# Kernel optimization log

Hardware: AMD Instinct MI355X
Metric: run time of the kernel (lower is better)

Reference implementation:

```python
import jax, jax.numpy as jnp
import numpy as np

B, N, T, E, H = 2, 512, 12, 128, 8
D = E // H  # head_dim = 16


def setup_inputs() -> dict:
    key = jax.random.key(0)
    ks = jax.random.split(key, 16)
    mk = lambda k, shape, s=1.0: (jax.random.normal(k, shape, dtype=jnp.float32) * s)
    inp = {
        'flow_q': mk(ks[0], (B, N, T, E)),
        'flow_k': mk(ks[1], (B, N, T, E)),
        'flow_v': mk(ks[2], (B, N, T, E)),
        'speed_q': mk(ks[3], (B, N, T, E)),
        'speed_k': mk(ks[4], (B, N, T, E)),
        'speed_v': mk(ks[5], (B, N, T, E)),
        # Linear weights stored as (in, out) so y = x @ W
        'WfQ': mk(ks[6], (E, E), 1.0 / np.sqrt(E)),
        'WfK': mk(ks[7], (E, E), 1.0 / np.sqrt(E)),
        'WfV': mk(ks[8], (E, E), 1.0 / np.sqrt(E)),
        'WsQ': mk(ks[9], (E, E), 1.0 / np.sqrt(E)),
        'WsK': mk(ks[10], (E, E), 1.0 / np.sqrt(E)),
        'WsV': mk(ks[11], (E, E), 1.0 / np.sqrt(E)),
        'Kj': mk(ks[12], (N, 1)),          # FlowSpeed params (xavier ~ small)
        'Vfp': mk(ks[13], (N, 1)),
        'Wout': mk(ks[14], (E, E), 1.0 / np.sqrt(E)),
        'bout': jnp.zeros((E,), dtype=jnp.float32),
    }
    return inp


def _heads(x, W):
    # [B,N,T,C] @ [C,E] -> [B,N,T,H,D] -> [B,H,T,N,D]
    y = jnp.einsum('bntc,ce->bnte', x, W).reshape(B, N, T, H, D)
    return jnp.transpose(y, (0, 3, 2, 1, 4))


def reference(flow_q, flow_k, flow_v, speed_q, speed_k, speed_v,
              WfQ, WfK, WfV, WsQ, WsK, WsV, Kj, Vfp, Wout, bout):
    Qf = _heads(flow_q, WfQ)
    Kf = _heads(flow_k, WfK)
    Vf = _heads(flow_v, WfV)
    Qs = _heads(speed_q, WsQ)
    Ks = _heads(speed_k, WsK)
    Vs = _heads(speed_v, WsV)

    scale = 1.0 / np.sqrt(D)
    # FlowSpeed nonlinearity on Qs; Kj/Vfp (N,1) broadcast over [B,H,T,N,D]
    Qf_from_speed = Kj * (Qs - Qs * Qs / (Vfp + 1e-05))

    att = lambda A, Bm: jax.nn.softmax(
        jnp.einsum('bhtnd,bhtmd->bhtnm', A, Bm) * scale, axis=-1)

    z_ff = att(Qf, Kf)
    z_fs = att(Kf, Qf_from_speed)
    z_sf = att(Ks, Qf)
    z_ss = att(Qs, Ks)

    ctx = lambda z, V: jnp.einsum('bhtnm,bhtmd->bhtnd', z, V)

    def proj_out(c):
        # [B,H,T,N,D] -> [B,N,T,H*D] -> fc_out
        c = jnp.transpose(c, (0, 3, 2, 1, 4)).reshape(B, N, T, E)
        return jnp.einsum('bnte,ef->bntf', c, Wout) + bout

    out_ff = proj_out(ctx(z_ff, Vf))
    out_fs = proj_out(ctx(z_fs, Vf))
    out_sf = proj_out(ctx(z_sf, Vs))
    out_ss = proj_out(ctx(z_ss, Vs))
    return (out_ff, out_fs, out_sf, out_ss)
```

## Files before the change

### kernel.cpp

```cpp
#include <hip/hip_runtime.h>
#include <math.h>

constexpr int Bb = 2, Nn = 512, Tt = 12, Ee = 128, Hh = 8, Dd = 16;
constexpr int NTOK   = Bb * Nn * Tt;
constexpr int PROJ   = NTOK * Ee;
constexpr int SLICES = Bb * Hh * Tt;
constexpr int NSL    = Nn * Dd;
constexpr long SLE   = (long)SLICES * NSL;
constexpr int NSL17  = 17 * 512;
constexpr long SLE17 = (long)SLICES * NSL17;


struct PtrPack { const float* x[6]; const float* W[6]; };
struct WPack   { const float* W[7]; };

typedef __attribute__((ext_vector_type(8)))  short bf16x8;
typedef __attribute__((ext_vector_type(16))) float f32x16;
union FragU { bf16x8 v; unsigned u[4]; };

__device__ __forceinline__ unsigned pk_bf16(float a, float b) {
  unsigned r;
  asm("v_cvt_pk_bf16_f32 %0, %1, %2" : "=v"(r) : "v"(a), "v"(b));
  return r;
}
__device__ __forceinline__ void split_frag(const float e[8], bf16x8& hv, bf16x8& lv) {
  FragU H, L;
  #pragma unroll
  for (int i = 0; i < 4; ++i) {
    const unsigned h = pk_bf16(e[2*i], e[2*i+1]);
    const float h0 = __uint_as_float(h << 16);
    const float h1 = __uint_as_float(h & 0xffff0000u);
    L.u[i] = pk_bf16(e[2*i] - h0, e[2*i+1] - h1);
    H.u[i] = h;
  }
  hv = H.v; lv = L.v;
}

__global__ __launch_bounds__(256) void prep_w_kernel(
    WPack wp, unsigned short* __restrict__ wf)
{
  const int m = blockIdx.x;
  const float SQ = sqrtf(0.25f * 1.4426950408889634f);
  const float scale = (m == 0 || m == 1 || m == 3 || m == 4) ? SQ : 1.0f;
  const float* __restrict__ W = wp.W[m];
  for (int e = threadIdx.x; e < 2048; e += 256) {
    const int ct = e >> 9, ks = (e >> 6) & 7, lane = e & 63;
    const int ql = lane & 31, hi = lane >> 5;
    const int c = ct * 32 + ql, k0 = ks * 16 + hi * 8;
    float w[8];
    #pragma unroll
    for (int j = 0; j < 8; ++j) w[j] = W[(size_t)(k0 + j) * Ee + c] * scale;
    bf16x8 hv, lv;
    split_frag(w, hv, lv);
    *(bf16x8*)&wf[((size_t)(m * 2 + 0) * 2048 + e) * 8] = hv;
    *(bf16x8*)&wf[((size_t)(m * 2 + 1) * 2048 + e) * 8] = lv;
  }
}

__global__ __launch_bounds__(256) void proj_mfma_kernel(
    PtrPack pp, const float* __restrict__ Kj, const float* __restrict__ Vfp,
    unsigned short* __restrict__ qk, unsigned short* __restrict__ vt,
    const unsigned short* __restrict__ wf)
{
  __shared__ float XS[32][132];
  const int ty = blockIdx.y;
  const int g  = blockIdx.x;
  const int nc = g & 15;
  const int bt = g >> 4;
  const int b  = bt / Tt, t = bt % Tt;
  const int n0 = nc * 32;
  const int tid = threadIdx.x;
  const int wave = tid >> 6, lane = tid & 63;
  const int ql = lane & 31, hi = lane >> 5;

  const float* __restrict__ xg = pp.x[ty];
  for (int i = tid; i < 1024; i += 256) {
    const int row = i >> 5, ch = i & 31;
    *(float4*)&XS[row][ch * 4] =
        *(const float4*)&xg[((size_t)(b * Nn + n0 + row) * Tt + t) * Ee + ch * 4];
  }
  __syncthreads();

  f32x16 acc;
  #pragma unroll
  for (int r = 0; r < 16; ++r) acc[r] = 0.f;

  const unsigned short* __restrict__ wbase =
      wf + ((size_t)(ty * 2) * 2048 + wave * 512 + lane) * 8;

  for (int ks = 0; ks < 8; ++ks) {
    float e8[8];
    *(float4*)&e8[0] = *(const float4*)&XS[ql][ks * 16 + hi * 8];
    *(float4*)&e8[4] = *(const float4*)&XS[ql][ks * 16 + hi * 8 + 4];
    bf16x8 xh, xl;
    split_frag(e8, xh, xl);
    const bf16x8 wh = *(const bf16x8*)&wbase[(size_t)ks * 512];
    const bf16x8 wl = *(const bf16x8*)&wbase[(size_t)ks * 512 + 2048 * 8];
    acc = __builtin_amdgcn_mfma_f32_32x32x16_bf16(xh, wh, acc, 0, 0, 0);
    acc = __builtin_amdgcn_mfma_f32_32x32x16_bf16(xh, wl, acc, 0, 0, 0);
    acc = __builtin_amdgcn_mfma_f32_32x32x16_bf16(xl, wh, acc, 0, 0, 0);
    if (ty == 3)
      acc = __builtin_amdgcn_mfma_f32_32x32x16_bf16(xl, wl, acc, 0, 0, 0);
  }
  __syncthreads();

  #pragma unroll
  for (int r = 0; r < 16; ++r)
    XS[(r & 3) + 8 * (r >> 2) + 4 * hi][wave * 32 + ql] = acc[r];
  __syncthreads();

  if (ty == 2 || ty == 5) {
    if (tid < 128) {
      const int h = tid >> 4, d = tid & 15;
      const int slice = (b * Hh + h) * Tt + t;
      const long vsel = (ty == 5);
      float v[32];
      #pragma unroll
      for (int n = 0; n < 32; ++n) v[n] = XS[n][h * 16 + d];
      FragU F[4];
      #pragma unroll
      for (int i = 0; i < 16; ++i)
        F[i >> 2].u[i & 3] = pk_bf16(v[2 * i], v[2 * i + 1]);
      unsigned short* __restrict__ dst =
          vt + vsel * SLE17 + (size_t)slice * NSL17 + d * 512 + n0;
      #pragma unroll
      for (int i = 0; i < 4; ++i) *(bf16x8*)&dst[i * 8] = F[i].v;
      if (d == 0) {
        FragU O_;
        #pragma unroll
        for (int i = 0; i < 4; ++i) O_.u[i] = 0x3F803F80u;
        unsigned short* __restrict__ op =
            vt + vsel * SLE17 + (size_t)slice * NSL17 + 16 * 512 + n0;
        #pragma unroll
        for (int i = 0; i < 4; ++i) *(bf16x8*)&op[i * 8] = O_.v;
      }
    }
  } else {
    const int h = tid >> 5, nn = tid & 31;
    const int slice = (b * Hh + h) * Tt + t;
    const int n = n0 + nn;
    float v[16];
    #pragma unroll
    for (int d = 0; d < 16; ++d) v[d] = XS[nn][h * 16 + d];
    FragU HI[2], LO[2];
    #pragma unroll
    for (int i = 0; i < 8; ++i) {
      const unsigned hw = pk_bf16(v[2 * i], v[2 * i + 1]);
      const float h0 = __uint_as_float(hw << 16);
      const float h1 = __uint_as_float(hw & 0xffff0000u);
      HI[i >> 2].u[i & 3] = hw;
      LO[i >> 2].u[i & 3] = pk_bf16(v[2 * i] - h0, v[2 * i + 1] - h1);
    }
    const int s = (ty == 0) ? 0 : (ty == 1) ? 1 : (ty == 3) ? 2 : 3;
    unsigned short* __restrict__ hp =
        qk + (size_t)(s * 2 + 0) * SLE + (size_t)slice * NSL + n * 16;
    unsigned short* __restrict__ lp =
        qk + (size_t)(s * 2 + 1) * SLE + (size_t)slice * NSL + n * 16;
    *(bf16x8*)&hp[0] = HI[0].v;  *(bf16x8*)&hp[8] = HI[1].v;
    *(bf16x8*)&lp[0] = LO[0].v;  *(bf16x8*)&lp[8] = LO[1].v;
    if (ty == 3) {
      const float SQ  = sqrtf(0.25f * 1.4426950408889634f);
      const float RSQ = 1.0f / SQ;
      const float kj = Kj[n];
      const float iv = 1.0f / (Vfp[n] + 1e-5f);
      float gv[16];
      #pragma unroll
      for (int d = 0; d < 16; ++d) {
        const float vq = v[d] * RSQ;
        gv[d] = SQ * (kj * (vq - vq * vq * iv));
      }
      FragU GH[2], GL[2];
      #pragma unroll
      for (int i = 0; i < 8; ++i) {
        const unsigned hw = pk_bf16(gv[2 * i], gv[2 * i + 1]);
        const float h0 = __uint_as_float(hw << 16);
        const float h1 = __uint_as_float(hw & 0xffff0000u);
        GH[i >> 2].u[i & 3] = hw;
        GL[i >> 2].u[i & 3] = pk_bf16(gv[2 * i] - h0, gv[2 * i + 1] - h1);
      }
      unsigned short* __restrict__ gp =
          qk + (size_t)(4 * 2 + 0) * SLE + (size_t)slice * NSL + n * 16;
      unsigned short* __restrict__ glp =
          qk + (size_t)(4 * 2 + 1) * SLE + (size_t)slice * NSL + n * 16;
      *(bf16x8*)&gp[0]  = GH[0].v;  *(bf16x8*)&gp[8]  = GH[1].v;
      *(bf16x8*)&glp[0] = GL[0].v;  *(bf16x8*)&glp[8] = GL[1].v;
    }
  }
}

__global__ __launch_bounds__(256) void attn_mfma_kernel(
    const unsigned short* __restrict__ qk, const unsigned short* __restrict__ vt,
    unsigned short* __restrict__ ctxh, unsigned short* __restrict__ ctxl)
{
  const int slice = blockIdx.x;
  const int ty    = blockIdx.y;
  const int a_s[4] = {0, 1, 3, 2};
  const int b_s[4] = {1, 4, 0, 3};
  const int v_s[4] = {0, 0, 1, 1};

  const unsigned short* __restrict__ Ah =
      qk + (size_t)(a_s[ty] * 2 + 0) * SLE + (size_t)slice * NSL;
  const unsigned short* __restrict__ Al =
      qk + (size_t)(a_s[ty] * 2 + 1) * SLE + (size_t)slice * NSL;
  const unsigned short* __restrict__ Kh_ =
      qk + (size_t)(b_s[ty] * 2 + 0) * SLE + (size_t)slice * NSL;
  const unsigned short* __restrict__ Kl_ =
      qk + (size_t)(b_s[ty] * 2 + 1) * SLE + (size_t)slice * NSL;
  const unsigned short* __restrict__ Vt_ =
      vt + (size_t)v_s[ty] * SLE17 + (size_t)slice * NSL17;

  const int tid  = threadIdx.x;
  const int wave = tid >> 6;
  const int lane = tid & 63;
  const int hi   = lane >> 5;
  const int ql   = lane & 31;
  const int q0   = blockIdx.z * 256 + wave * 64;
  const int dv   = (ql < 16) ? ql : 16;
  const unsigned short* __restrict__ vbase = Vt_ + dv * 512;

  bf16x8 qh[2], qlo[2];
  #pragma unroll
  for (int qt = 0; qt < 2; ++qt) {
    const int qrow = q0 + qt * 32 + ql;
    qh[qt]  = *(const bf16x8*)&Ah[qrow * 16 + hi * 8];
    qlo[qt] = *(const bf16x8*)&Al[qrow * 16 + hi * 8];
  }

  f32x16 Z;
  #pragma unroll
  for (int r = 0; r < 16; ++r) Z[r] = 0.0f;

  f32x16 o[2];
  float  m_[2] = {-1e30f, -1e30f};
  #pragma unroll
  for (int qt = 0; qt < 2; ++qt)
    #pragma unroll
    for (int r = 0; r < 16; ++r) o[qt][r] = 0.0f;

  for (int kc = 0; kc < Nn; kc += 32) {
    const int krow = kc + ql;
    const bf16x8 kh = *(const bf16x8*)&Kh_[krow * 16 + hi * 8];
    const bf16x8 kl = *(const bf16x8*)&Kl_[krow * 16 + hi * 8];
    const bf16x8 vb0 = *(const bf16x8*)&vbase[kc + hi * 8];
    const bf16x8 vb1 = *(const bf16x8*)&vbase[kc + 16 + hi * 8];

    #pragma unroll
    for (int qt = 0; qt < 2; ++qt) {
      f32x16 S;
      S = __builtin_amdgcn_mfma_f32_32x32x16_bf16(kh, qh[qt],  Z, 0, 0, 0);
      S = __builtin_amdgcn_mfma_f32_32x32x16_bf16(kh, qlo[qt], S, 0, 0, 0);
      S = __builtin_amdgcn_mfma_f32_32x32x16_bf16(kl, qh[qt],  S, 0, 0, 0);
      if (ty == 1)
        S = __builtin_amdgcn_mfma_f32_32x32x16_bf16(kl, qlo[qt], S, 0, 0, 0);

      float p[16];
      if (ty == 1) {
        float smax = S[0];
        #pragma unroll
        for (int r = 1; r < 16; ++r) smax = fmaxf(smax, S[r]);
        float cm = fmaxf(smax, __shfl_xor(smax, 32));
        if (!__all(cm <= m_[qt] + 8.0f)) {
          const float nm = fmaxf(m_[qt], cm);
          const float f  = __builtin_amdgcn_exp2f(m_[qt] - nm);
          #pragma unroll
          for (int r = 0; r < 16; ++r) {
            const int qloc = (r & 3) + 8 * (r >> 2) + 4 * hi;
            o[qt][r] *= __shfl(f, qloc);
          }
          m_[qt] = nm;
        }
        #pragma unroll
        for (int r = 0; r < 16; ++r)
          p[r] = __builtin_amdgcn_exp2f(S[r] - m_[qt]);
      } else {
        #pragma unroll
        for (int r = 0; r < 16; ++r)
          p[r] = __builtin_amdgcn_exp2f(S[r]);
      }

      FragU pa0, pa1;
      {
        unsigned wa = pk_bf16(p[0],  p[1]);
        unsigned wb = pk_bf16(p[2],  p[3]);
        unsigned wc = pk_bf16(p[4],  p[5]);
        unsigned wd = pk_bf16(p[6],  p[7]);
        asm("v_permlane32_swap_b32 %0, %1" : "+v"(wa), "+v"(wc));
        asm("v_permlane32_swap_b32 %0, %1" : "+v"(wb), "+v"(wd));
        pa0.u[0] = wa; pa0.u[1] = wb; pa0.u[2] = wc; pa0.u[3] = wd;
        unsigned we = pk_bf16(p[8],  p[9]);
        unsigned wg = pk_bf16(p[10], p[11]);
        unsigned wi = pk_bf16(p[12], p[13]);
        unsigned wj = pk_bf16(p[14], p[15]);
        asm("v_permlane32_swap_b32 %0, %1" : "+v"(we), "+v"(wi));
        asm("v_permlane32_swap_b32 %0, %1" : "+v"(wg), "+v"(wj));
        pa1.u[0] = we; pa1.u[1] = wg; pa1.u[2] = wi; pa1.u[3] = wj;
      }
      o[qt] = __builtin_amdgcn_mfma_f32_32x32x16_bf16(pa0.v, vb0, o[qt], 0, 0, 0);
      o[qt] = __builtin_amdgcn_mfma_f32_32x32x16_bf16(pa1.v, vb1, o[qt], 0, 0, 0);
    }
  }

  const int b = slice / (Hh * Tt);
  const int h = (slice / Tt) % Hh;
  const int t = slice % Tt;
  unsigned short* __restrict__ ch = ctxh + (size_t)ty * PROJ;
  unsigned short* __restrict__ cl = ctxl + (size_t)ty * PROJ;
  const int lsrc = (lane & 32) | 16;
  #pragma unroll
  for (int qt = 0; qt < 2; ++qt) {
    #pragma unroll
    for (int r = 0; r < 16; ++r) {
      const int qloc = (r & 3) + 8 * (r >> 2) + 4 * hi;
      const float lsum = __shfl(o[qt][r], lsrc);
      if (ql < 16) {
        const int n = q0 + qt * 32 + qloc;
        const float val = o[qt][r] * __builtin_amdgcn_rcpf(lsum);
        const unsigned hv = pk_bf16(val, val);
        const float hf = __uint_as_float(hv << 16);
        const unsigned lv = pk_bf16(val - hf, val - hf);
        const size_t off = (((size_t)b * Nn + n) * Tt + t) * Ee + h * Dd + ql;
        ch[off] = (unsigned short)hv;
        cl[off] = (unsigned short)lv;
      }
    }
  }
}

__global__ __launch_bounds__(256) void out_mfma_kernel(
    const unsigned short* __restrict__ ctxh, const unsigned short* __restrict__ ctxl,
    const unsigned short* __restrict__ wf, const float* __restrict__ bout,
    float* __restrict__ out)
{
  const int ty   = blockIdx.y;
  const int tok0 = blockIdx.x * 32;
  const int wave = threadIdx.x >> 6, lane = threadIdx.x & 63;
  const int ql = lane & 31, hi = lane >> 5;

  f32x16 acc;
  #pragma unroll
  for (int r = 0; r < 16; ++r) acc[r] = 0.f;

  const unsigned short* __restrict__ xh_row =
      ctxh + (size_t)ty * PROJ + (size_t)(tok0 + ql) * Ee;
  const unsigned short* __restrict__ xl_row =
      ctxl + (size_t)ty * PROJ + (size_t)(tok0 + ql) * Ee;
  const unsigned short* __restrict__ wbase =
      wf + ((size_t)(6 * 2) * 2048 + wave * 512 + lane) * 8;

  for (int ks = 0; ks < 8; ++ks) {
    const bf16x8 xh = *(const bf16x8*)&xh_row[ks * 16 + hi * 8];
    const bf16x8 xl = *(const bf16x8*)&xl_row[ks * 16 + hi * 8];
    const bf16x8 wh = *(const bf16x8*)&wbase[(size_t)ks * 512];
    const bf16x8 wl = *(const bf16x8*)&wbase[(size_t)ks * 512 + 2048 * 8];
    acc = __builtin_amdgcn_mfma_f32_32x32x16_bf16(xh, wh, acc, 0, 0, 0);
    acc = __builtin_amdgcn_mfma_f32_32x32x16_bf16(xh, wl, acc, 0, 0, 0);
    acc = __builtin_amdgcn_mfma_f32_32x32x16_bf16(xl, wh, acc, 0, 0, 0);
  }

  const int c = wave * 32 + ql;
  const float bc = bout[c];
  float* __restrict__ dst = out + (size_t)ty * PROJ;
  #pragma unroll
  for (int r = 0; r < 16; ++r) {
    const int tok = tok0 + (r & 3) + 8 * (r >> 2) + 4 * hi;
    dst[(size_t)tok * Ee + c] = acc[r] + bc;
  }
}

extern "C" void kernel_launch(void* const* d_in, const int* in_sizes, int n_in,
                              void* d_out, int out_size, void* d_ws, size_t ws_size,
                              hipStream_t stream) {
  const float* fq  = (const float*)d_in[0];
  const float* fk  = (const float*)d_in[1];
  const float* fv  = (const float*)d_in[2];
  const float* sq  = (const float*)d_in[3];
  const float* sk  = (const float*)d_in[4];
  const float* sv  = (const float*)d_in[5];
  const float* WfQ = (const float*)d_in[6];
  const float* WfK = (const float*)d_in[7];
  const float* WfV = (const float*)d_in[8];
  const float* WsQ = (const float*)d_in[9];
  const float* WsK = (const float*)d_in[10];
  const float* WsV = (const float*)d_in[11];
  const float* Kj  = (const float*)d_in[12];
  const float* Vfp = (const float*)d_in[13];
  const float* Wout = (const float*)d_in[14];
  const float* bout = (const float*)d_in[15];

  unsigned short* qk   = (unsigned short*)d_ws;
  unsigned short* vt   = qk + (size_t)10 * SLE;
  unsigned short* wf   = vt + (size_t)2 * SLE17;
  unsigned short* ctxh = wf + 229376;
  unsigned short* ctxl = ctxh + (size_t)4 * PROJ;

  PtrPack pp;
  pp.x[0] = fq; pp.x[1] = fk; pp.x[2] = fv;
  pp.x[3] = sq; pp.x[4] = sk; pp.x[5] = sv;
  pp.W[0] = WfQ; pp.W[1] = WfK; pp.W[2] = WfV;
  pp.W[3] = WsQ; pp.W[4] = WsK; pp.W[5] = WsV;
  WPack wp;
  wp.W[0] = WfQ; wp.W[1] = WfK; wp.W[2] = WfV;
  wp.W[3] = WsQ; wp.W[4] = WsK; wp.W[5] = WsV; wp.W[6] = Wout;

  prep_w_kernel<<<7, 256, 0, stream>>>(wp, wf);
  proj_mfma_kernel<<<dim3(384, 6), 256, 0, stream>>>(pp, Kj, Vfp, qk, vt, wf);
  attn_mfma_kernel<<<dim3(SLICES, 4, 2), 256, 0, stream>>>(qk, vt, ctxh, ctxl);
  out_mfma_kernel<<<dim3(NTOK / 32, 4), 256, 0, stream>>>(ctxh, ctxl, wf, bout, (float*)d_out);
}
```

Before: 206.1 us.

## Fuse attention and output projection via shared-memory context tile

Merges the attention kernel and the output-projection kernel. Each block now covers all 8 heads for one (b,t) and 64 queries, with one head per wave. The normalized context goes into a shared-memory tile and is multiplied by Wout inside the same kernel, which removes the global write and re-read of the context buffers and one launch. It also drops the low-order bf16 split of the context, so the projection uses 2 MFMAs instead of 3, at some cost in accuracy. The grid is smaller (768 blocks of 512 threads), which may reduce parallelism in the attention phase.

Measured after the change: 190.2 us. -7.7%, faster.

```diff
diff --git a/kernel.cpp b/kernel.cpp
--- a/kernel.cpp
+++ b/kernel.cpp
@@ -188,15 +188,28 @@
   }
 }
 
-__global__ __launch_bounds__(256) void attn_mfma_kernel(
+__global__ __launch_bounds__(512) void attn_out_kernel(
     const unsigned short* __restrict__ qk, const unsigned short* __restrict__ vt,
-    unsigned short* __restrict__ ctxh, unsigned short* __restrict__ ctxl)
+    const unsigned short* __restrict__ wf, const float* __restrict__ bout,
+    float* __restrict__ out)
 {
-  const int slice = blockIdx.x;
-  const int ty    = blockIdx.y;
+  __shared__ unsigned short XH[64][136];
+  const int bt = blockIdx.x;
+  const int b  = bt / Tt, t = bt % Tt;
+  const int ty = blockIdx.y;
+  const int q0 = blockIdx.z * 64;
+
   const int a_s[4] = {0, 1, 3, 2};
   const int b_s[4] = {1, 4, 0, 3};
   const int v_s[4] = {0, 0, 1, 1};
+
+  const int tid  = threadIdx.x;
+  const int wave = tid >> 6;
+  const int lane = tid & 63;
+  const int hi   = lane >> 5;
+  const int ql   = lane & 31;
+  const int h    = wave;
+  const int slice = (b * Hh + h) * Tt + t;
 
   const unsigned short* __restrict__ Ah =
       qk + (size_t)(a_s[ty] * 2 + 0) * SLE + (size_t)slice * NSL;
@@ -209,13 +222,7 @@
   const unsigned short* __restrict__ Vt_ =
       vt + (size_t)v_s[ty] * SLE17 + (size_t)slice * NSL17;
 
-  const int tid  = threadIdx.x;
-  const int wave = tid >> 6;
-  const int lane = tid & 63;
-  const int hi   = lane >> 5;
-  const int ql   = lane & 31;
-  const int q0   = blockIdx.z * 256 + wave * 64;
-  const int dv   = (ql < 16) ? ql : 16;
+  const int dv = (ql < 16) ? ql : 16;
   const unsigned short* __restrict__ vbase = Vt_ + dv * 512;
 
   bf16x8 qh[2], qlo[2];
@@ -300,11 +307,6 @@
     }
   }
 
-  const int b = slice / (Hh * Tt);
-  const int h = (slice / Tt) % Hh;
-  const int t = slice % Tt;
-  unsigned short* __restrict__ ch = ctxh + (size_t)ty * PROJ;
-  unsigned short* __restrict__ cl = ctxl + (size_t)ty * PROJ;
   const int lsrc = (lane & 32) | 16;
   #pragma unroll
   for (int qt = 0; qt < 2; ++qt) {
@@ -313,57 +315,38 @@
       const int qloc = (r & 3) + 8 * (r >> 2) + 4 * hi;
       const float lsum = __shfl(o[qt][r], lsrc);
       if (ql < 16) {
-        const int n = q0 + qt * 32 + qloc;
         const float val = o[qt][r] * __builtin_amdgcn_rcpf(lsum);
-        const unsigned hv = pk_bf16(val, val);
-        const float hf = __uint_as_float(hv << 16);
-        const unsigned lv = pk_bf16(val - hf, val - hf);
-        const size_t off = (((size_t)b * Nn + n) * Tt + t) * Ee + h * Dd + ql;
-        ch[off] = (unsigned short)hv;
-        cl[off] = (unsigned short)lv;
-      }
-    }
-  }
-}
-
-__global__ __launch_bounds__(256) void out_mfma_kernel(
-    const unsigned short* __restrict__ ctxh, const unsigned short* __restrict__ ctxl,
-    const unsigned short* __restrict__ wf, const float* __restrict__ bout,
-    float* __restrict__ out)
-{
-  const int ty   = blockIdx.y;
-  const int tok0 = blockIdx.x * 32;
-  const int wave = threadIdx.x >> 6, lane = threadIdx.x & 63;
-  const int ql = lane & 31, hi = lane >> 5;
-
+        XH[qt * 32 + qloc][h * 16 + ql] =
+            (unsigned short)(pk_bf16(val, val) & 0xffffu);
+      }
+    }
+  }
+  __syncthreads();
+
+  const int tt = wave >> 2, ct = wave & 3;
   f32x16 acc;
   #pragma unroll
   for (int r = 0; r < 16; ++r) acc[r] = 0.f;
 
-  const unsigned short* __restrict__ xh_row =
-      ctxh + (size_t)ty * PROJ + (size_t)(tok0 + ql) * Ee;
-  const unsigned short* __restrict__ xl_row =
-      ctxl + (size_t)ty * PROJ + (size_t)(tok0 + ql) * Ee;
   const unsigned short* __restrict__ wbase =
-      wf + ((size_t)(6 * 2) * 2048 + wave * 512 + lane) * 8;
+      wf + ((size_t)(6 * 2) * 2048 + ct * 512 + lane) * 8;
 
   for (int ks = 0; ks < 8; ++ks) {
-    const bf16x8 xh = *(const bf16x8*)&xh_row[ks * 16 + hi * 8];
-    const bf16x8 xl = *(const bf16x8*)&xl_row[ks * 16 + hi * 8];
+    const bf16x8 xh = *(const bf16x8*)&XH[tt * 32 + ql][ks * 16 + hi * 8];
     const bf16x8 wh = *(const bf16x8*)&wbase[(size_t)ks * 512];
     const bf16x8 wl = *(const bf16x8*)&wbase[(size_t)ks * 512 + 2048 * 8];
     acc = __builtin_amdgcn_mfma_f32_32x32x16_bf16(xh, wh, acc, 0, 0, 0);
     acc = __builtin_amdgcn_mfma_f32_32x32x16_bf16(xh, wl, acc, 0, 0, 0);
-    acc = __builtin_amdgcn_mfma_f32_32x32x16_bf16(xl, wh, acc, 0, 0, 0);
-  }
-
-  const int c = wave * 32 + ql;
+  }
+
+  const int c = ct * 32 + ql;
   const float bc = bout[c];
   float* __restrict__ dst = out + (size_t)ty * PROJ;
   #pragma unroll
   for (int r = 0; r < 16; ++r) {
-    const int tok = tok0 + (r & 3) + 8 * (r >> 2) + 4 * hi;
-    dst[(size_t)tok * Ee + c] = acc[r] + bc;
+    const int n = q0 + tt * 32 + (r & 3) + 8 * (r >> 2) + 4 * hi;
+    const size_t tok = ((size_t)b * Nn + n) * Tt + t;
+    dst[tok * Ee + c] = acc[r] + bc;
   }
 }
 
@@ -387,11 +370,9 @@
   const float* Wout = (const float*)d_in[14];
   const float* bout = (const float*)d_in[15];
 
-  unsigned short* qk   = (unsigned short*)d_ws;
-  unsigned short* vt   = qk + (size_t)10 * SLE;
-  unsigned short* wf   = vt + (size_t)2 * SLE17;
-  unsigned short* ctxh = wf + 229376;
-  unsigned short* ctxl = ctxh + (size_t)4 * PROJ;
+  unsigned short* qk = (unsigned short*)d_ws;
+  unsigned short* vt = qk + (size_t)10 * SLE;
+  unsigned short* wf = vt + (size_t)2 * SLE17;
 
   PtrPack pp;
   pp.x[0] = fq; pp.x[1] = fk; pp.x[2] = fv;
@@ -404,6 +385,5 @@
 
   prep_w_kernel<<<7, 256, 0, stream>>>(wp, wf);
   proj_mfma_kernel<<<dim3(384, 6), 256, 0, stream>>>(pp, Kj, Vfp, qk, vt, wf);
-  attn_mfma_kernel<<<dim3(SLICES, 4, 2), 256, 0, stream>>>(qk, vt, ctxh, ctxl);
-  out_mfma_kernel<<<dim3(NTOK / 32, 4), 256, 0, stream>>>(ctxh, ctxl, wf, bout, (float*)d_out);
-}
+  attn_out_kernel<<<dim3(24, 4, 8), 512, 0, stream>>>(qk, vt, wf, bout, (float*)d_out);
+}
```
